# Optimization experiments

Measured on AMD Instinct MI355X. Metric: run time of the kernel, lower is better.

The kernel has to match this reference:

```python
import jax, jax.numpy as jnp
import numpy as np

DIM = 768
H = 12
D = DIM // H  # head_dim = 64
SCALE = D ** -0.5


def _split_heads(x):
    # [b, n, h*d] -> [b, h, n, d]
    b, n, _ = x.shape
    return x.reshape(b, n, H, D).transpose(0, 2, 1, 3)


def setup_inputs() -> dict:
    key = jax.random.key(0)
    ks = jax.random.split(key, 16)
    B, NQ, NKV = 2, 2048, 2048
    w_init = lambda k: jax.random.normal(k, (DIM, DIM), dtype=jnp.float32) * 0.02
    return {
        "words": jax.random.normal(ks[0], (B, NQ, DIM), dtype=jnp.float32),
        "position_words": jax.random.normal(ks[1], (B, NQ, DIM), dtype=jnp.float32),
        "conscious_words": jax.random.normal(ks[2], (B, NQ, DIM), dtype=jnp.float32),
        "cross_kv": jax.random.normal(ks[3], (B, NKV, DIM), dtype=jnp.float32),
        "position_cross": jax.random.normal(ks[4], (B, NKV, DIM), dtype=jnp.float32),
        "Wq_w": w_init(ks[5]), "Wk_w": w_init(ks[6]), "Wv_w": w_init(ks[7]),
        "Wq_p": w_init(ks[8]), "Wk_p": w_init(ks[9]),
        "Wq_c": w_init(ks[10]), "Wk_c": w_init(ks[11]),
        "latent_k": jax.random.normal(ks[12], (DIM,), dtype=jnp.float32),
        "Wo": w_init(ks[13]),
        "bo": jnp.zeros((DIM,), dtype=jnp.float32),
    }


def reference(words, position_words, conscious_words, cross_kv, position_cross,
              Wq_w, Wk_w, Wv_w, Wq_p, Wk_p, Wq_c, Wk_c, latent_k, Wo, bo):
    # Queries from three sources. Sum of the 9 pairwise QK^T scores equals
    # (sum of Qs) @ (sum of Ks)^T by bilinearity of matmul (same math as source).
    q = _split_heads(words @ Wq_w) + _split_heads(position_words @ Wq_p) \
        + _split_heads(conscious_words @ Wq_c)        # [b,h,nq,d]
    # latent conscious key: same vector for every kv position
    kc = (latent_k @ Wk_c).reshape(H, D)              # [h,d]
    k = _split_heads(cross_kv @ Wk_w) + _split_heads(position_cross @ Wk_p) \
        + kc[None, :, None, :]                        # [b,h,nkv,d]
    v = _split_heads(cross_kv @ Wv_w)                 # [b,h,nkv,d]

    score = jnp.einsum('bhid,bhjd->bhij', q, k) * SCALE  # [b,h,nq,nkv]
    attn = jax.nn.softmax(score, axis=-1)
    out = jnp.einsum('bhij,bhjd->bhid', attn, v)      # [b,h,nq,d]
    b, _, nq, _ = out.shape
    out = out.transpose(0, 2, 1, 3).reshape(b, nq, H * D)
    return out @ Wo + bo
```

## Files before the change

### kernel.cpp

```cpp
#include <hip/hip_runtime.h>
#include <math.h>

#define DIM  768
#define NH   12
#define HD   64
#define NQ   2048
#define NKV  2048
#define QSC_LOG2E 0.18033688011112042f

typedef short bf16x8  __attribute__((ext_vector_type(8)));
typedef float f32x4   __attribute__((ext_vector_type(4)));
typedef float f32x16  __attribute__((ext_vector_type(16)));

__device__ __forceinline__ unsigned short f2bf(float f) {
    unsigned u = __float_as_uint(f);
    unsigned r = (u + 0x7FFFu + ((u >> 16) & 1u)) >> 16;
    return (unsigned short)r;
}
__device__ __forceinline__ float bf2f(unsigned short u) {
    return __uint_as_float(((unsigned)u) << 16);
}

__device__ __forceinline__ unsigned cvtpk_bf16(float a, float b) {
    unsigned r;
    asm("v_cvt_pk_bf16_f32 %0, %1, %2" : "=v"(r) : "v"(a), "v"(b));
    return r;
}

__device__ __forceinline__ void plswap(unsigned& a, unsigned& b) {
    asm("v_permlane32_swap_b32 %0, %1" : "+v"(a), "+v"(b));
}

__device__ __forceinline__ float vexp2f(float x) {
#if __has_builtin(__builtin_amdgcn_exp2f)
    return __builtin_amdgcn_exp2f(x);
#else
    float r;
    asm("v_exp_f32 %0, %1\ns_nop 0" : "=v"(r) : "v"(x));
    return r;
#endif
}

__device__ __forceinline__ void ld_lds16(void* lds, const void* g) {
    __builtin_amdgcn_global_load_lds(
        (const __attribute__((address_space(1))) unsigned int*)g,
        (__attribute__((address_space(3))) unsigned int*)lds, 16, 0, 0);
}

__device__ __forceinline__ f32x16 z16() {
    f32x16 r;
    #pragma unroll
    for (int e = 0; e < 16; ++e) r[e] = 0.f;
    return r;
}

union PB16 { unsigned u[4]; bf16x8 v; };

__global__ __launch_bounds__(256)
void prep_kernel(const float* __restrict__ w0, const float* __restrict__ w1,
                 const float* __restrict__ w2, const float* __restrict__ w3,
                 const float* __restrict__ w4, const float* __restrict__ w5,
                 const float* __restrict__ w6, unsigned short* __restrict__ wt,
                 const float* __restrict__ latent, const float* __restrict__ Wkc,
                 float* __restrict__ kc) {
    __shared__ float t[32][33];
    int bid = blockIdx.x;
    if (bid < 4032) {
        int iz = bid / 576, rem = bid - iz * 576;
        int iy = rem / 24, ix = rem - iy * 24;
        const float* Ws[7] = {w0, w1, w2, w3, w4, w5, w6};
        const float* W = Ws[iz];
        unsigned short* D = wt + (size_t)iz * (768 * 768);
        int r0 = iy * 32, c0 = ix * 32;
        int tx = threadIdx.x & 31, ty = threadIdx.x >> 5;
        #pragma unroll
        for (int yy = 0; yy < 4; ++yy)
            t[ty * 4 + yy][tx] = W[(size_t)(r0 + ty * 4 + yy) * 768 + c0 + tx];
        __syncthreads();
        #pragma unroll
        for (int yy = 0; yy < 4; ++yy)
            D[(size_t)(c0 + ty * 4 + yy) * 768 + r0 + tx] = f2bf(t[tx][ty * 4 + yy]);
    } else {
        int jb = bid - 4032;
        float (&red)[16][17] = *reinterpret_cast<float(*)[16][17]>(&t[0][0]);
        int tx = threadIdx.x & 15, ty = threadIdx.x >> 4;
        int j = jb * 16 + tx;
        float acc = 0.f;
        for (int i = ty * 48; i < ty * 48 + 48; ++i)
            acc += latent[i] * Wkc[i * DIM + j];
        red[ty][tx] = acc;
        __syncthreads();
        if (ty == 0) {
            float s = 0.f;
            #pragma unroll
            for (int k = 0; k < 16; ++k) s += red[k][tx];
            kc[j] = s;
        }
    }
}

struct QCfg {
    const float* A0; const float* A1; const float* A2;
    const unsigned short* B0; const unsigned short* B1; const unsigned short* B2;
    const float* bias; float scale; void* out; int npair; int mode;
};

__global__ __launch_bounds__(256)
void gemm_qvk(QCfg c0, QCfg c1, QCfg c2) {
    __shared__ unsigned short As[2][64 * 64];
    __shared__ unsigned short Bs[2][128 * 64];
    const int tid = threadIdx.x;
    const int w = tid >> 6, l = tid & 63, g = l >> 4, r16 = l & 15;

    int p = blockIdx.x;
    int xcd = p & 7, s = p >> 3;
    int bx = s % 6, gg = s / 6;
    int gidx = gg * 8 + xcd;
    int by = gidx & 63, z = gidx >> 6;
    const int n0 = bx * 128, m0 = by * 64;

    QCfg c = (z == 0) ? c0 : (z == 1) ? c1 : c2;
    const float* Alist[3] = {c.A0, c.A1, c.A2};
    const unsigned short* Blist[3] = {c.B0, c.B1, c.B2};

    const int ar = tid >> 2, ac = (tid & 3) * 16;
    const int aswz = (ar & 7) << 4;
    float4 av0, av1, av2, av3;

    f32x4 acc[4][2];
    #pragma unroll
    for (int i = 0; i < 4; ++i)
        #pragma unroll
        for (int j = 0; j < 2; ++j) acc[i][j] = (f32x4){0.f, 0.f, 0.f, 0.f};

#define ALOAD(AP, K0) { \
    const float* _ap = (AP) + (size_t)(m0 + ar) * 768 + (K0) + ac; \
    av0 = *(const float4*)_ap;       av1 = *(const float4*)(_ap + 4); \
    av2 = *(const float4*)(_ap + 8); av3 = *(const float4*)(_ap + 12); }

#define AWRITE(BUFI) { \
    uint4 u0_, u1_; \
    u0_.x = cvtpk_bf16(av0.x, av0.y); u0_.y = cvtpk_bf16(av0.z, av0.w); \
    u0_.z = cvtpk_bf16(av1.x, av1.y); u0_.w = cvtpk_bf16(av1.z, av1.w); \
    u1_.x = cvtpk_bf16(av2.x, av2.y); u1_.y = cvtpk_bf16(av2.z, av2.w); \
    u1_.z = cvtpk_bf16(av3.x, av3.y); u1_.w = cvtpk_bf16(av3.z, av3.w); \
    *(uint4*)((char*)As[BUFI] + ar * 128 + ((2 * ac) ^ aswz)) = u0_; \
    *(uint4*)((char*)As[BUFI] + ar * 128 + ((2 * ac + 16) ^ aswz)) = u1_; }

#define BSTAGE(BUFI, BP, K0) { _Pragma("unroll") \
    for (int is = 0; is < 4; ++is) { \
        int u = is * 256 + tid, r = u >> 3, cc = u & 7; \
        int col = ((cc ^ (r & 7)) << 3); \
        ld_lds16((char*)Bs[BUFI] + is * 4096 + w * 1024, \
                 (BP) + (size_t)(n0 + r) * 768 + (K0) + col); } }

    const int NSTEPS = c.npair * 12;
    int pn = 0, kn = 0;
    ALOAD(Alist[0], 0);
    BSTAGE(0, Blist[0], 0);
    AWRITE(0);
    kn = 64;
    __syncthreads();

    #pragma unroll 1
    for (int st = 0; st < NSTEPS; ++st) {
        int cur = st & 1;
        bool pre = (st + 1 < NSTEPS);
        if (pre) {
            ALOAD(Alist[pn], kn);
            BSTAGE(cur ^ 1, Blist[pn], kn);
        }
        const char* Ab = (const char*)As[cur];
        const char* Bb = (const char*)Bs[cur];
        #pragma unroll
        for (int kk = 0; kk < 2; ++kk) {
            bf16x8 af[4], bf[2];
            #pragma unroll
            for (int i = 0; i < 4; ++i) {
                int row = i * 16 + r16;
                af[i] = *(const bf16x8*)(Ab + row * 128 +
                          ((kk * 64 + g * 16) ^ ((row & 7) << 4)));
            }
            #pragma unroll
            for (int j = 0; j < 2; ++j) {
                int row = w * 32 + j * 16 + r16;
                bf[j] = *(const bf16x8*)(Bb + row * 128 +
                          ((kk * 64 + g * 16) ^ ((row & 7) << 4)));
            }
            #pragma unroll
            for (int i = 0; i < 4; ++i)
                #pragma unroll
                for (int j = 0; j < 2; ++j)
                    acc[i][j] = __builtin_amdgcn_mfma_f32_16x16x32_bf16(
                        af[i], bf[j], acc[i][j], 0, 0, 0);
        }
        if (pre) {
            AWRITE(cur ^ 1);
            kn += 64; if (kn == 768) { kn = 0; ++pn; }
        }
        __syncthreads();
    }
#undef ALOAD
#undef AWRITE
#undef BSTAGE

    const int mode = c.mode;
    #pragma unroll
    for (int i = 0; i < 4; ++i) {
        #pragma unroll
        for (int j = 0; j < 2; ++j) {
            int col = n0 + w * 32 + j * 16 + r16;
            float bv = (mode == 0 && c.bias) ? c.bias[col] : 0.f;
            #pragma unroll
            for (int rr = 0; rr < 4; ++rr) {
                int row = m0 + i * 16 + g * 4 + rr;
                float v = acc[i][j][rr];
                if (mode == 2) v *= c.scale;
                v += bv;
                if (mode == 3) {
                    int bb = row >> 11, q = row & 2047;
                    ((unsigned short*)c.out)[(size_t)(bb * 768 + col) * 2048 + q] = f2bf(v);
                } else {
                    ((unsigned short*)c.out)[(size_t)row * 768 + col] = f2bf(v);
                }
            }
        }
    }
}

__global__ __launch_bounds__(256)
void gemm_out(const unsigned short* __restrict__ A,
              const unsigned short* __restrict__ B,
              const float* __restrict__ bias, float* __restrict__ Cout) {
    __shared__ unsigned short As[2][64 * 64];
    __shared__ unsigned short Bs[2][128 * 64];
    const int tid = threadIdx.x;
    const int w = tid >> 6, l = tid & 63, g = l >> 4, r16 = l & 15;

    int o_lin = blockIdx.x;
    int wl = (o_lin & 7) * 48 + (o_lin >> 3);
    int bx = wl % 6, by = wl / 6;
    const int n0 = bx * 128, m0 = by * 64;

    f32x4 acc[4][2];
    #pragma unroll
    for (int i = 0; i < 4; ++i)
        #pragma unroll
        for (int j = 0; j < 2; ++j) acc[i][j] = (f32x4){0.f, 0.f, 0.f, 0.f};

#define GSTAGE(BUFI, K0) { \
    _Pragma("unroll") \
    for (int is = 0; is < 2; ++is) { \
        int u = is * 256 + tid, r = u >> 3, cc = u & 7; \
        int col = ((cc ^ (r & 7)) << 3); \
        ld_lds16((char*)As[BUFI] + is * 4096 + w * 1024, \
                 A + (size_t)(m0 + r) * 768 + (K0) + col); } \
    _Pragma("unroll") \
    for (int is = 0; is < 4; ++is) { \
        int u = is * 256 + tid, r = u >> 3, cc = u & 7; \
        int col = ((cc ^ (r & 7)) << 3); \
        ld_lds16((char*)Bs[BUFI] + is * 4096 + w * 1024, \
                 B + (size_t)(n0 + r) * 768 + (K0) + col); } }

    GSTAGE(0, 0);
    __syncthreads();

    #pragma unroll 1
    for (int st = 0; st < 12; ++st) {
        int cur = st & 1;
        if (st + 1 < 12) GSTAGE(cur ^ 1, (st + 1) * 64);
        const char* Ab = (const char*)As[cur];
        const char* Bb = (const char*)Bs[cur];
        #pragma unroll
        for (int kk = 0; kk < 2; ++kk) {
            bf16x8 af[4], bf[2];
            #pragma unroll
            for (int i = 0; i < 4; ++i) {
                int row = i * 16 + r16;
                af[i] = *(const bf16x8*)(Ab + row * 128 +
                          ((kk * 64 + g * 16) ^ ((row & 7) << 4)));
            }
            #pragma unroll
            for (int j = 0; j < 2; ++j) {
                int row = w * 32 + j * 16 + r16;
                bf[j] = *(const bf16x8*)(Bb + row * 128 +
                          ((kk * 64 + g * 16) ^ ((row & 7) << 4)));
            }
            #pragma unroll
            for (int i = 0; i < 4; ++i)
                #pragma unroll
                for (int j = 0; j < 2; ++j)
                    acc[i][j] = __builtin_amdgcn_mfma_f32_16x16x32_bf16(
                        af[i], bf[j], acc[i][j], 0, 0, 0);
        }
        __syncthreads();
    }
#undef GSTAGE

    #pragma unroll
    for (int i = 0; i < 4; ++i) {
        #pragma unroll
        for (int j = 0; j < 2; ++j) {
            int col = n0 + w * 32 + j * 16 + r16;
            float bv = bias[col];
            #pragma unroll
            for (int rr = 0; rr < 4; ++rr) {
                int row = m0 + i * 16 + g * 4 + rr;
                Cout[(size_t)row * 768 + col] = acc[i][j][rr] + bv;
            }
        }
    }
}

__global__ __launch_bounds__(256)
void flash2(const unsigned short* __restrict__ Qb,
            const unsigned short* __restrict__ Kb,
            const unsigned short* __restrict__ Vt,
            unsigned short* __restrict__ P0, unsigned short* __restrict__ P1,
            unsigned short* __restrict__ P2, unsigned short* __restrict__ P3,
            float2* __restrict__ ML) {
    __shared__ unsigned short KV[2][2][4096];
    const int tid = threadIdx.x;
    const int w = tid >> 6, l = tid & 63, lo = l & 31, hi = l >> 5;

    int p = blockIdx.x + 64 * blockIdx.y;
    int xcd = p & 7, s = p >> 3;
    int gg = s >> 6, inner = s & 63;
    int bh = gg * 8 + xcd;
    int qi = inner >> 2, part = inner & 3;
    int b = bh / NH, h = bh % NH;
    int q0 = qi * 128;
    int kvbase = part * 512;

    bf16x8 qf[4];
    {
        const unsigned short* Qrow =
            Qb + (size_t)(b * NQ + q0 + w * 32 + lo) * DIM + h * HD + hi * 8;
        #pragma unroll
        for (int kc = 0; kc < 4; ++kc) qf[kc] = *(const bf16x8*)(Qrow + kc * 16);
    }

    f32x16 o0 = z16(), o1 = z16();
    float m = -3.0e38f, lsum = 0.f;

    const unsigned short* Kbase = Kb + (size_t)(b * NKV) * DIM + h * HD;
    const unsigned short* Vbase = Vt + ((size_t)b * DIM + h * HD) * NKV;

#define FSTAGE(BUFI, T0) { \
    _Pragma("unroll") \
    for (int is = 0; is < 2; ++is) { \
        int u = is * 256 + tid, r = u >> 3, cc = u & 7; \
        int col = ((cc ^ (r & 7)) << 3); \
        ld_lds16((char*)KV[BUFI][0] + is * 4096 + w * 1024, \
                 Kbase + (size_t)((T0) + r) * 768 + col); \
        ld_lds16((char*)KV[BUFI][1] + is * 4096 + w * 1024, \
                 Vbase + (size_t)r * 2048 + (T0) + col); } }

    FSTAGE(0, kvbase);
    __syncthreads();

    #pragma unroll 1
    for (int t = 0; t < 8; ++t) {
        int cur = t & 1;
        if (t < 7) FSTAGE(cur ^ 1, kvbase + (t + 1) * 64);

        const char* Kp = (const char*)KV[cur][0];
        const char* Vp = (const char*)KV[cur][1];

        f32x16 s0 = z16(), s1 = z16();
        __builtin_amdgcn_s_setprio(1);
        #pragma unroll
        for (int kc = 0; kc < 4; ++kc) {
            int r0 = lo, r1 = 32 + lo;
            bf16x8 k0 = *(const bf16x8*)(Kp + r0 * 128 +
                          ((kc * 32 + hi * 16) ^ ((r0 & 7) << 4)));
            bf16x8 k1 = *(const bf16x8*)(Kp + r1 * 128 +
                          ((kc * 32 + hi * 16) ^ ((r1 & 7) << 4)));
            s0 = __builtin_amdgcn_mfma_f32_32x32x16_bf16(k0, qf[kc], s0, 0, 0, 0);
            s1 = __builtin_amdgcn_mfma_f32_32x32x16_bf16(k1, qf[kc], s1, 0, 0, 0);
        }
        __builtin_amdgcn_s_setprio(0);

        float a8[8];
        #pragma unroll
        for (int e = 0; e < 8; ++e)
            a8[e] = fmaxf(fmaxf(fmaxf(s0[e], s0[e + 8]), s1[e]), s1[e + 8]);
        float pm = fmaxf(fmaxf(fmaxf(fmaxf(a8[0], a8[1]), fmaxf(a8[2], a8[3])),
                               fmaxf(fmaxf(a8[4], a8[5]), fmaxf(a8[6], a8[7]))), -3.0e38f);
        pm = fmaxf(pm, __shfl_xor(pm, 32));

        if (__any(pm > m + 10.f)) {
            float mn = fmaxf(m, pm);
            float sc = vexp2f(m - mn);
            lsum *= sc;
            #pragma unroll
            for (int e = 0; e < 16; ++e) { o0[e] *= sc; o1[e] *= sc; }
            m = mn;
        }

        #pragma unroll
        for (int e = 0; e < 16; ++e) {
            s0[e] = vexp2f(s0[e] - m);
            s1[e] = vexp2f(s1[e] - m);
        }

        float b8[8];
        #pragma unroll
        for (int e = 0; e < 8; ++e)
            b8[e] = (s0[e] + s0[e + 8]) + (s1[e] + s1[e + 8]);
        float rs = ((b8[0] + b8[1]) + (b8[2] + b8[3])) +
                   ((b8[4] + b8[5]) + (b8[6] + b8[7]));
        rs += __shfl_xor(rs, 32);
        lsum += rs;

        PB16 pb[4];
        #pragma unroll
        for (int cc = 0; cc < 2; ++cc) {
            unsigned a0 = cvtpk_bf16(s0[cc * 8 + 0], s0[cc * 8 + 1]);
            unsigned a1 = cvtpk_bf16(s0[cc * 8 + 2], s0[cc * 8 + 3]);
            unsigned b0 = cvtpk_bf16(s0[cc * 8 + 4], s0[cc * 8 + 5]);
            unsigned b1 = cvtpk_bf16(s0[cc * 8 + 6], s0[cc * 8 + 7]);
            plswap(a0, b0);
            plswap(a1, b1);
            pb[cc].u[0] = a0; pb[cc].u[1] = a1; pb[cc].u[2] = b0; pb[cc].u[3] = b1;
            unsigned c0 = cvtpk_bf16(s1[cc * 8 + 0], s1[cc * 8 + 1]);
            unsigned c1 = cvtpk_bf16(s1[cc * 8 + 2], s1[cc * 8 + 3]);
            unsigned d0 = cvtpk_bf16(s1[cc * 8 + 4], s1[cc * 8 + 5]);
            unsigned d1 = cvtpk_bf16(s1[cc * 8 + 6], s1[cc * 8 + 7]);
            plswap(c0, d0);
            plswap(c1, d1);
            pb[2 + cc].u[0] = c0; pb[2 + cc].u[1] = c1;
            pb[2 + cc].u[2] = d0; pb[2 + cc].u[3] = d1;
        }

        __builtin_amdgcn_s_setprio(1);
        #pragma unroll
        for (int c = 0; c < 4; ++c) {
            int r0 = lo, r1 = 32 + lo;
            bf16x8 v0 = *(const bf16x8*)(Vp + r0 * 128 +
                          ((c * 32 + hi * 16) ^ ((r0 & 7) << 4)));
            bf16x8 v1 = *(const bf16x8*)(Vp + r1 * 128 +
                          ((c * 32 + hi * 16) ^ ((r1 & 7) << 4)));
            o0 = __builtin_amdgcn_mfma_f32_32x32x16_bf16(v0, pb[c].v, o0, 0, 0, 0);
            o1 = __builtin_amdgcn_mfma_f32_32x32x16_bf16(v1, pb[c].v, o1, 0, 0, 0);
        }
        __builtin_amdgcn_s_setprio(0);
        __syncthreads();
    }
#undef FSTAGE

    unsigned short* Pp = (part == 0) ? P0 : (part == 1) ? P1 : (part == 2) ? P2 : P3;
    const int q = q0 + w * 32 + lo;
    unsigned short* Op = Pp + ((size_t)bh * 2048 + q) * 64;
    #pragma unroll
    for (int grp = 0; grp < 4; ++grp) {
        int r0 = grp * 4;
        int d0 = grp * 8 + 4 * hi;
        uint2 v0, v1;
        v0.x = cvtpk_bf16(o0[r0 + 0], o0[r0 + 1]);
        v0.y = cvtpk_bf16(o0[r0 + 2], o0[r0 + 3]);
        *(uint2*)(Op + d0) = v0;
        v1.x = cvtpk_bf16(o1[r0 + 0], o1[r0 + 1]);
        v1.y = cvtpk_bf16(o1[r0 + 2], o1[r0 + 3]);
        *(uint2*)(Op + 32 + d0) = v1;
    }
    if (hi == 0)
        ML[(size_t)(part * 24 + bh) * 2048 + q] = make_float2(m, lsum);
}

__global__ __launch_bounds__(256)
void combine4(const unsigned short* __restrict__ P0, const unsigned short* __restrict__ P1,
              const unsigned short* __restrict__ P2, const unsigned short* __restrict__ P3,
              const float2* __restrict__ ML, unsigned short* __restrict__ AO) {
    int bh = blockIdx.y;
    int idx = blockIdx.x * 256 + threadIdx.x;
    int q = idx >> 1, dh = (idx & 1) * 32;

    float2 u0 = ML[(size_t)(0 * 24 + bh) * 2048 + q];
    float2 u1 = ML[(size_t)(1 * 24 + bh) * 2048 + q];
    float2 u2 = ML[(size_t)(2 * 24 + bh) * 2048 + q];
    float2 u3 = ML[(size_t)(3 * 24 + bh) * 2048 + q];
    float M = fmaxf(fmaxf(u0.x, u1.x), fmaxf(u2.x, u3.x));
    float w0 = vexp2f(u0.x - M), w1 = vexp2f(u1.x - M);
    float w2 = vexp2f(u2.x - M), w3 = vexp2f(u3.x - M);
    float inv = 1.f / (w0 * u0.y + w1 * u1.y + w2 * u2.y + w3 * u3.y);
    w0 *= inv; w1 *= inv; w2 *= inv; w3 *= inv;

    size_t off = ((size_t)bh * 2048 + q) * 64 + dh;
    float acc[32];
    #pragma unroll
    for (int e = 0; e < 32; ++e) acc[e] = 0.f;
    const unsigned short* Ps[4] = {P0, P1, P2, P3};
    float ws[4] = {w0, w1, w2, w3};
    #pragma unroll
    for (int pp = 0; pp < 4; ++pp) {
        const unsigned short* src = Ps[pp] + off;
        float wv = ws[pp];
        #pragma unroll
        for (int c = 0; c < 4; ++c) {
            ushort4 hh2;
            uint4 vv = *(const uint4*)(src + c * 8);
            unsigned uu[4] = {vv.x, vv.y, vv.z, vv.w};
            #pragma unroll
            for (int e = 0; e < 4; ++e) {
                acc[c * 8 + e * 2 + 0] += wv * bf2f((unsigned short)(uu[e] & 0xFFFF));
                acc[c * 8 + e * 2 + 1] += wv * bf2f((unsigned short)(uu[e] >> 16));
            }
            (void)hh2;
        }
    }
    int b = bh / NH, h = bh % NH;
    unsigned short* dst = AO + ((size_t)(b * 2048 + q)) * DIM + h * HD + dh;
    #pragma unroll
    for (int c = 0; c < 4; ++c) {
        uint4 ov;
        ov.x = cvtpk_bf16(acc[c * 8 + 0], acc[c * 8 + 1]);
        ov.y = cvtpk_bf16(acc[c * 8 + 2], acc[c * 8 + 3]);
        ov.z = cvtpk_bf16(acc[c * 8 + 4], acc[c * 8 + 5]);
        ov.w = cvtpk_bf16(acc[c * 8 + 6], acc[c * 8 + 7]);
        *(uint4*)(dst + c * 8) = ov;
    }
}

extern "C" void kernel_launch(void* const* d_in, const int* in_sizes, int n_in,
                              void* d_out, int out_size, void* d_ws, size_t ws_size,
                              hipStream_t stream) {
    const float* words   = (const float*)d_in[0];
    const float* posw    = (const float*)d_in[1];
    const float* consc   = (const float*)d_in[2];
    const float* cross   = (const float*)d_in[3];
    const float* pcross  = (const float*)d_in[4];
    const float* Wq_w    = (const float*)d_in[5];
    const float* Wk_w    = (const float*)d_in[6];
    const float* Wv_w    = (const float*)d_in[7];
    const float* Wq_p    = (const float*)d_in[8];
    const float* Wk_p    = (const float*)d_in[9];
    const float* Wq_c    = (const float*)d_in[10];
    const float* Wk_c    = (const float*)d_in[11];
    const float* latentk = (const float*)d_in[12];
    const float* Wo      = (const float*)d_in[13];
    const float* bo      = (const float*)d_in[14];

    char* arena = (char*)d_ws;
    const size_t WTE = 768 * 768;
    unsigned short* WT = (unsigned short*)(arena);
    unsigned short* QB = (unsigned short*)(arena + 8257536);
    unsigned short* VT = (unsigned short*)(arena + 14548992);
    unsigned short* KB = (unsigned short*)(arena + 20840448);
    unsigned short* P0 = (unsigned short*)(arena + 27131904);
    unsigned short* P1 = (unsigned short*)(arena + 33423360);
    unsigned short* P2 = (unsigned short*)(arena + 39714816);
    unsigned short* P3 = (unsigned short*)(arena);
    float2* ML         = (float2*)(arena + 46006272);
    float* KCV         = (float*)(arena + 47579136);

    prep_kernel<<<dim3(4080), dim3(256), 0, stream>>>(
        Wq_w, Wq_p, Wq_c, Wk_w, Wk_p, Wv_w, Wo, WT, latentk, Wk_c, KCV);

    QCfg cq = { words, posw, consc,
                WT + 0 * WTE, WT + 1 * WTE, WT + 2 * WTE,
                nullptr, QSC_LOG2E, QB, 3, 2 };
    QCfg cv = { cross, nullptr, nullptr,
                WT + 5 * WTE, nullptr, nullptr,
                nullptr, 1.f, VT, 1, 3 };
    QCfg ck = { cross, pcross, nullptr,
                WT + 3 * WTE, WT + 4 * WTE, nullptr,
                KCV, 1.f, KB, 2, 0 };
    gemm_qvk<<<dim3(1152), dim3(256), 0, stream>>>(cq, cv, ck);

    flash2<<<dim3(64, 24), dim3(256), 0, stream>>>(QB, KB, VT, P0, P1, P2, P3, ML);

    combine4<<<dim3(16, 24), dim3(256), 0, stream>>>(P0, P1, P2, P3, ML, QB);

    gemm_out<<<dim3(384), dim3(256), 0, stream>>>(QB, WT + 6 * WTE, bo, (float*)d_out);
}
```

Baseline: 140.0 us.

## Enlarge projection GEMM tiles to 128x128 and drop LDS double buffering

Both the QKV projection and output projection GEMMs now use 128x128 block tiles, with a 2x2 wave arrangement where each wave computes a 64x64 sub-tile. This halves the block count and raises MFMA work per LDS load. Double buffering is replaced by single-buffered load/sync/compute steps with launch bounds set for occupancy 3. The mode-3 transposed V store is vectorised into uint2 writes. The trade-off is less load/compute overlap inside a block and fewer blocks per GPU (576 and 192), which risks underfilling the CUs.

After: 186.0 us. 32.8% more time.

```diff
diff --git a/kernel.cpp b/kernel.cpp
--- a/kernel.cpp
+++ b/kernel.cpp
@@ -105,209 +105,201 @@
     const float* bias; float scale; void* out; int npair; int mode;
 };
 
-__global__ __launch_bounds__(256)
+__global__ __launch_bounds__(256, 3)
 void gemm_qvk(QCfg c0, QCfg c1, QCfg c2) {
-    __shared__ unsigned short As[2][64 * 64];
-    __shared__ unsigned short Bs[2][128 * 64];
+    __shared__ unsigned short As[128 * 64];
+    __shared__ unsigned short Bs[128 * 64];
     const int tid = threadIdx.x;
     const int w = tid >> 6, l = tid & 63, g = l >> 4, r16 = l & 15;
+    const int wr = w >> 1, wc = w & 1;
 
     int p = blockIdx.x;
     int xcd = p & 7, s = p >> 3;
     int bx = s % 6, gg = s / 6;
     int gidx = gg * 8 + xcd;
-    int by = gidx & 63, z = gidx >> 6;
-    const int n0 = bx * 128, m0 = by * 64;
+    int by = gidx & 31, z = gidx >> 5;
+    const int n0 = bx * 128, m0 = by * 128;
 
     QCfg c = (z == 0) ? c0 : (z == 1) ? c1 : c2;
     const float* Alist[3] = {c.A0, c.A1, c.A2};
     const unsigned short* Blist[3] = {c.B0, c.B1, c.B2};
 
-    const int ar = tid >> 2, ac = (tid & 3) * 16;
+    const int ar = tid >> 1, ac = (tid & 1) * 32;
     const int aswz = (ar & 7) << 4;
-    float4 av0, av1, av2, av3;
-
-    f32x4 acc[4][2];
+
+    f32x4 acc[4][4];
     #pragma unroll
     for (int i = 0; i < 4; ++i)
         #pragma unroll
-        for (int j = 0; j < 2; ++j) acc[i][j] = (f32x4){0.f, 0.f, 0.f, 0.f};
-
-#define ALOAD(AP, K0) { \
-    const float* _ap = (AP) + (size_t)(m0 + ar) * 768 + (K0) + ac; \
-    av0 = *(const float4*)_ap;       av1 = *(const float4*)(_ap + 4); \
-    av2 = *(const float4*)(_ap + 8); av3 = *(const float4*)(_ap + 12); }
-
-#define AWRITE(BUFI) { \
-    uint4 u0_, u1_; \
-    u0_.x = cvtpk_bf16(av0.x, av0.y); u0_.y = cvtpk_bf16(av0.z, av0.w); \
-    u0_.z = cvtpk_bf16(av1.x, av1.y); u0_.w = cvtpk_bf16(av1.z, av1.w); \
-    u1_.x = cvtpk_bf16(av2.x, av2.y); u1_.y = cvtpk_bf16(av2.z, av2.w); \
-    u1_.z = cvtpk_bf16(av3.x, av3.y); u1_.w = cvtpk_bf16(av3.z, av3.w); \
-    *(uint4*)((char*)As[BUFI] + ar * 128 + ((2 * ac) ^ aswz)) = u0_; \
-    *(uint4*)((char*)As[BUFI] + ar * 128 + ((2 * ac + 16) ^ aswz)) = u1_; }
-
-#define BSTAGE(BUFI, BP, K0) { _Pragma("unroll") \
-    for (int is = 0; is < 4; ++is) { \
-        int u = is * 256 + tid, r = u >> 3, cc = u & 7; \
-        int col = ((cc ^ (r & 7)) << 3); \
-        ld_lds16((char*)Bs[BUFI] + is * 4096 + w * 1024, \
-                 (BP) + (size_t)(n0 + r) * 768 + (K0) + col); } }
+        for (int j = 0; j < 4; ++j) acc[i][j] = (f32x4){0.f, 0.f, 0.f, 0.f};
 
     const int NSTEPS = c.npair * 12;
     int pn = 0, kn = 0;
-    ALOAD(Alist[0], 0);
-    BSTAGE(0, Blist[0], 0);
-    AWRITE(0);
-    kn = 64;
-    __syncthreads();
 
     #pragma unroll 1
     for (int st = 0; st < NSTEPS; ++st) {
-        int cur = st & 1;
-        bool pre = (st + 1 < NSTEPS);
-        if (pre) {
-            ALOAD(Alist[pn], kn);
-            BSTAGE(cur ^ 1, Blist[pn], kn);
-        }
-        const char* Ab = (const char*)As[cur];
-        const char* Bb = (const char*)Bs[cur];
+        const float* Ap = Alist[pn] + (size_t)(m0 + ar) * 768 + kn + ac;
+        float4 av0 = *(const float4*)(Ap + 0);
+        float4 av1 = *(const float4*)(Ap + 4);
+        float4 av2 = *(const float4*)(Ap + 8);
+        float4 av3 = *(const float4*)(Ap + 12);
+        float4 av4 = *(const float4*)(Ap + 16);
+        float4 av5 = *(const float4*)(Ap + 20);
+        float4 av6 = *(const float4*)(Ap + 24);
+        float4 av7 = *(const float4*)(Ap + 28);
+        __syncthreads();
+        {
+            uint4 u0, u1, u2, u3;
+            u0.x = cvtpk_bf16(av0.x, av0.y); u0.y = cvtpk_bf16(av0.z, av0.w);
+            u0.z = cvtpk_bf16(av1.x, av1.y); u0.w = cvtpk_bf16(av1.z, av1.w);
+            u1.x = cvtpk_bf16(av2.x, av2.y); u1.y = cvtpk_bf16(av2.z, av2.w);
+            u1.z = cvtpk_bf16(av3.x, av3.y); u1.w = cvtpk_bf16(av3.z, av3.w);
+            u2.x = cvtpk_bf16(av4.x, av4.y); u2.y = cvtpk_bf16(av4.z, av4.w);
+            u2.z = cvtpk_bf16(av5.x, av5.y); u2.w = cvtpk_bf16(av5.z, av5.w);
+            u3.x = cvtpk_bf16(av6.x, av6.y); u3.y = cvtpk_bf16(av6.z, av6.w);
+            u3.z = cvtpk_bf16(av7.x, av7.y); u3.w = cvtpk_bf16(av7.z, av7.w);
+            char* dst = (char*)As + ar * 128;
+            *(uint4*)(dst + ((2 * ac + 0)  ^ aswz)) = u0;
+            *(uint4*)(dst + ((2 * ac + 16) ^ aswz)) = u1;
+            *(uint4*)(dst + ((2 * ac + 32) ^ aswz)) = u2;
+            *(uint4*)(dst + ((2 * ac + 48) ^ aswz)) = u3;
+        }
+        {
+            const unsigned short* Bp = Blist[pn];
+            #pragma unroll
+            for (int is = 0; is < 4; ++is) {
+                int u = is * 256 + tid, r = u >> 3, cc = u & 7;
+                int col = ((cc ^ (r & 7)) << 3);
+                ld_lds16((char*)Bs + is * 4096 + w * 1024,
+                         Bp + (size_t)(n0 + r) * 768 + kn + col);
+            }
+        }
+        __syncthreads();
+
         #pragma unroll
         for (int kk = 0; kk < 2; ++kk) {
-            bf16x8 af[4], bf[2];
+            bf16x8 af[4], bf[4];
             #pragma unroll
             for (int i = 0; i < 4; ++i) {
-                int row = i * 16 + r16;
-                af[i] = *(const bf16x8*)(Ab + row * 128 +
+                int row = wr * 64 + i * 16 + r16;
+                af[i] = *(const bf16x8*)((const char*)As + row * 128 +
                           ((kk * 64 + g * 16) ^ ((row & 7) << 4)));
             }
             #pragma unroll
-            for (int j = 0; j < 2; ++j) {
-                int row = w * 32 + j * 16 + r16;
-                bf[j] = *(const bf16x8*)(Bb + row * 128 +
+            for (int j = 0; j < 4; ++j) {
+                int row = wc * 64 + j * 16 + r16;
+                bf[j] = *(const bf16x8*)((const char*)Bs + row * 128 +
                           ((kk * 64 + g * 16) ^ ((row & 7) << 4)));
             }
             #pragma unroll
             for (int i = 0; i < 4; ++i)
                 #pragma unroll
-                for (int j = 0; j < 2; ++j)
+                for (int j = 0; j < 4; ++j)
                     acc[i][j] = __builtin_amdgcn_mfma_f32_16x16x32_bf16(
                         af[i], bf[j], acc[i][j], 0, 0, 0);
         }
-        if (pre) {
-            AWRITE(cur ^ 1);
-            kn += 64; if (kn == 768) { kn = 0; ++pn; }
-        }
-        __syncthreads();
-    }
-#undef ALOAD
-#undef AWRITE
-#undef BSTAGE
+        kn += 64; if (kn == 768) { kn = 0; ++pn; }
+    }
 
     const int mode = c.mode;
     #pragma unroll
     for (int i = 0; i < 4; ++i) {
         #pragma unroll
-        for (int j = 0; j < 2; ++j) {
-            int col = n0 + w * 32 + j * 16 + r16;
-            float bv = (mode == 0 && c.bias) ? c.bias[col] : 0.f;
-            #pragma unroll
-            for (int rr = 0; rr < 4; ++rr) {
-                int row = m0 + i * 16 + g * 4 + rr;
-                float v = acc[i][j][rr];
-                if (mode == 2) v *= c.scale;
-                v += bv;
-                if (mode == 3) {
-                    int bb = row >> 11, q = row & 2047;
-                    ((unsigned short*)c.out)[(size_t)(bb * 768 + col) * 2048 + q] = f2bf(v);
-                } else {
-                    ((unsigned short*)c.out)[(size_t)row * 768 + col] = f2bf(v);
+        for (int j = 0; j < 4; ++j) {
+            int col = n0 + wc * 64 + j * 16 + r16;
+            int row0 = m0 + wr * 64 + i * 16 + g * 4;
+            if (mode == 3) {
+                int bb = row0 >> 11, q = row0 & 2047;
+                uint2 v;
+                v.x = cvtpk_bf16(acc[i][j][0], acc[i][j][1]);
+                v.y = cvtpk_bf16(acc[i][j][2], acc[i][j][3]);
+                *(uint2*)((unsigned short*)c.out +
+                          (size_t)(bb * 768 + col) * 2048 + q) = v;
+            } else {
+                float bv = (mode == 0 && c.bias) ? c.bias[col] : 0.f;
+                #pragma unroll
+                for (int rr = 0; rr < 4; ++rr) {
+                    float v = acc[i][j][rr];
+                    if (mode == 2) v *= c.scale;
+                    v += bv;
+                    ((unsigned short*)c.out)[(size_t)(row0 + rr) * 768 + col] = f2bf(v);
                 }
             }
         }
     }
 }
 
-__global__ __launch_bounds__(256)
+__global__ __launch_bounds__(256, 3)
 void gemm_out(const unsigned short* __restrict__ A,
               const unsigned short* __restrict__ B,
               const float* __restrict__ bias, float* __restrict__ Cout) {
-    __shared__ unsigned short As[2][64 * 64];
-    __shared__ unsigned short Bs[2][128 * 64];
+    __shared__ unsigned short As[128 * 64];
+    __shared__ unsigned short Bs[128 * 64];
     const int tid = threadIdx.x;
     const int w = tid >> 6, l = tid & 63, g = l >> 4, r16 = l & 15;
-
-    int o_lin = blockIdx.x;
-    int wl = (o_lin & 7) * 48 + (o_lin >> 3);
-    int bx = wl % 6, by = wl / 6;
-    const int n0 = bx * 128, m0 = by * 64;
-
-    f32x4 acc[4][2];
+    const int wr = w >> 1, wc = w & 1;
+
+    int p = blockIdx.x;
+    int xcd = p & 7, s = p >> 3;
+    int bx = s % 6;
+    int by = (s / 6) * 8 + xcd;
+    const int n0 = bx * 128, m0 = by * 128;
+
+    f32x4 acc[4][4];
     #pragma unroll
     for (int i = 0; i < 4; ++i)
         #pragma unroll
-        for (int j = 0; j < 2; ++j) acc[i][j] = (f32x4){0.f, 0.f, 0.f, 0.f};
-
-#define GSTAGE(BUFI, K0) { \
-    _Pragma("unroll") \
-    for (int is = 0; is < 2; ++is) { \
-        int u = is * 256 + tid, r = u >> 3, cc = u & 7; \
-        int col = ((cc ^ (r & 7)) << 3); \
-        ld_lds16((char*)As[BUFI] + is * 4096 + w * 1024, \
-                 A + (size_t)(m0 + r) * 768 + (K0) + col); } \
-    _Pragma("unroll") \
-    for (int is = 0; is < 4; ++is) { \
-        int u = is * 256 + tid, r = u >> 3, cc = u & 7; \
-        int col = ((cc ^ (r & 7)) << 3); \
-        ld_lds16((char*)Bs[BUFI] + is * 4096 + w * 1024, \
-                 B + (size_t)(n0 + r) * 768 + (K0) + col); } }
-
-    GSTAGE(0, 0);
-    __syncthreads();
+        for (int j = 0; j < 4; ++j) acc[i][j] = (f32x4){0.f, 0.f, 0.f, 0.f};
 
     #pragma unroll 1
     for (int st = 0; st < 12; ++st) {
-        int cur = st & 1;
-        if (st + 1 < 12) GSTAGE(cur ^ 1, (st + 1) * 64);
-        const char* Ab = (const char*)As[cur];
-        const char* Bb = (const char*)Bs[cur];
+        int k0 = st * 64;
+        __syncthreads();
+        #pragma unroll
+        for (int is = 0; is < 4; ++is) {
+            int u = is * 256 + tid, r = u >> 3, cc = u & 7;
+            int col = ((cc ^ (r & 7)) << 3);
+            ld_lds16((char*)As + is * 4096 + w * 1024,
+                     A + (size_t)(m0 + r) * 768 + k0 + col);
+            ld_lds16((char*)Bs + is * 4096 + w * 1024,
+                     B + (size_t)(n0 + r) * 768 + k0 + col);
+        }
+        __syncthreads();
+
         #pragma unroll
         for (int kk = 0; kk < 2; ++kk) {
-            bf16x8 af[4], bf[2];
+            bf16x8 af[4], bf[4];
             #pragma unroll
             for (int i = 0; i < 4; ++i) {
-                int row = i * 16 + r16;
-                af[i] = *(const bf16x8*)(Ab + row * 128 +
+                int row = wr * 64 + i * 16 + r16;
+                af[i] = *(const bf16x8*)((const char*)As + row * 128 +
                           ((kk * 64 + g * 16) ^ ((row & 7) << 4)));
             }
             #pragma unroll
-            for (int j = 0; j < 2; ++j) {
-                int row = w * 32 + j * 16 + r16;
-                bf[j] = *(const bf16x8*)(Bb + row * 128 +
+            for (int j = 0; j < 4; ++j) {
+                int row = wc * 64 + j * 16 + r16;
+                bf[j] = *(const bf16x8*)((const char*)Bs + row * 128 +
                           ((kk * 64 + g * 16) ^ ((row & 7) << 4)));
             }
             #pragma unroll
             for (int i = 0; i < 4; ++i)
                 #pragma unroll
-                for (int j = 0; j < 2; ++j)
+                for (int j = 0; j < 4; ++j)
                     acc[i][j] = __builtin_amdgcn_mfma_f32_16x16x32_bf16(
                         af[i], bf[j], acc[i][j], 0, 0, 0);
         }
-        __syncthreads();
-    }
-#undef GSTAGE
+    }
 
     #pragma unroll
     for (int i = 0; i < 4; ++i) {
         #pragma unroll
-        for (int j = 0; j < 2; ++j) {
-            int col = n0 + w * 32 + j * 16 + r16;
+        for (int j = 0; j < 4; ++j) {
+            int col = n0 + wc * 64 + j * 16 + r16;
             float bv = bias[col];
-            #pragma unroll
-            for (int rr = 0; rr < 4; ++rr) {
-                int row = m0 + i * 16 + g * 4 + rr;
-                Cout[(size_t)row * 768 + col] = acc[i][j][rr] + bv;
-            }
+            int row0 = m0 + wr * 64 + i * 16 + g * 4;
+            #pragma unroll
+            for (int rr = 0; rr < 4; ++rr)
+                Cout[(size_t)(row0 + rr) * 768 + col] = acc[i][j][rr] + bv;
         }
     }
 }
@@ -385,8 +377,8 @@
         #pragma unroll
         for (int e = 0; e < 8; ++e)
             a8[e] = fmaxf(fmaxf(fmaxf(s0[e], s0[e + 8]), s1[e]), s1[e + 8]);
-        float pm = fmaxf(fmaxf(fmaxf(fmaxf(a8[0], a8[1]), fmaxf(a8[2], a8[3])),
-                               fmaxf(fmaxf(a8[4], a8[5]), fmaxf(a8[6], a8[7]))), -3.0e38f);
+        float pm = fmaxf(fmaxf(fmaxf(a8[0], a8[1]), fmaxf(a8[2], a8[3])),
+                         fmaxf(fmaxf(a8[4], a8[5]), fmaxf(a8[6], a8[7])));
         pm = fmaxf(pm, __shfl_xor(pm, 32));
 
         if (__any(pm > m + 10.f)) {
@@ -498,7 +490,6 @@
         float wv = ws[pp];
         #pragma unroll
         for (int c = 0; c < 4; ++c) {
-            ushort4 hh2;
             uint4 vv = *(const uint4*)(src + c * 8);
             unsigned uu[4] = {vv.x, vv.y, vv.z, vv.w};
             #pragma unroll
@@ -506,7 +497,6 @@
                 acc[c * 8 + e * 2 + 0] += wv * bf2f((unsigned short)(uu[e] & 0xFFFF));
                 acc[c * 8 + e * 2 + 1] += wv * bf2f((unsigned short)(uu[e] >> 16));
             }
-            (void)hh2;
         }
     }
     int b = bh / NH, h = bh % NH;
@@ -566,11 +556,11 @@
     QCfg ck = { cross, pcross, nullptr,
                 WT + 3 * WTE, WT + 4 * WTE, nullptr,
                 KCV, 1.f, KB, 2, 0 };
-    gemm_qvk<<<dim3(1152), dim3(256), 0, stream>>>(cq, cv, ck);
+    gemm_qvk<<<dim3(576), dim3(256), 0, stream>>>(cq, cv, ck);
 
     flash2<<<dim3(64, 24), dim3(256), 0, stream>>>(QB, KB, VT, P0, P1, P2, P3, ML);
 
     combine4<<<dim3(16, 24), dim3(256), 0, stream>>>(P0, P1, P2, P3, ML, QB);
 
-    gemm_out<<<dim3(384), dim3(256), 0, stream>>>(QB, WT + 6 * WTE, bo, (float*)d_out);
-}
+    gemm_out<<<dim3(192), dim3(256), 0, stream>>>(QB, WT + 6 * WTE, bo, (float*)d_out);
+}
```

## Restructure QKV projection GEMM main loop into unrolled two-stage pipeline with explicit waits

Applied to the files above, without the earlier changes.

The QKV projection GEMM loop is rewritten as a manually unrolled pair of steps. The fp32 A tiles now load into two alternating register sets, so A can be fetched one extra step ahead. The single __syncthreads is replaced with fine-grained s_waitcnt vmcnt/lgkmcnt plus s_barrier, so some outstanding global loads can stay in flight across the barrier. A launch-bounds occupancy hint of 3 is added, and a redundant clamp in the attention max reduction is dropped. The trade-offs are more registers for the duplicate A buffers and reliance on hand-counted vmcnt values being correct.

After: 142.1 us, median of 3. About the same (+1.5%).

```diff
diff --git a/kernel.cpp b/kernel.cpp
--- a/kernel.cpp
+++ b/kernel.cpp
@@ -105,7 +105,7 @@
     const float* bias; float scale; void* out; int npair; int mode;
 };
 
-__global__ __launch_bounds__(256)
+__global__ __launch_bounds__(256, 3)
 void gemm_qvk(QCfg c0, QCfg c1, QCfg c2) {
     __shared__ unsigned short As[2][64 * 64];
     __shared__ unsigned short Bs[2][128 * 64];
@@ -125,7 +125,6 @@
 
     const int ar = tid >> 2, ac = (tid & 3) * 16;
     const int aswz = (ar & 7) << 4;
-    float4 av0, av1, av2, av3;
 
     f32x4 acc[4][2];
     #pragma unroll
@@ -133,76 +132,96 @@
         #pragma unroll
         for (int j = 0; j < 2; ++j) acc[i][j] = (f32x4){0.f, 0.f, 0.f, 0.f};
 
-#define ALOAD(AP, K0) { \
-    const float* _ap = (AP) + (size_t)(m0 + ar) * 768 + (K0) + ac; \
-    av0 = *(const float4*)_ap;       av1 = *(const float4*)(_ap + 4); \
-    av2 = *(const float4*)(_ap + 8); av3 = *(const float4*)(_ap + 12); }
-
-#define AWRITE(BUFI) { \
-    uint4 u0_, u1_; \
-    u0_.x = cvtpk_bf16(av0.x, av0.y); u0_.y = cvtpk_bf16(av0.z, av0.w); \
-    u0_.z = cvtpk_bf16(av1.x, av1.y); u0_.w = cvtpk_bf16(av1.z, av1.w); \
-    u1_.x = cvtpk_bf16(av2.x, av2.y); u1_.y = cvtpk_bf16(av2.z, av2.w); \
-    u1_.z = cvtpk_bf16(av3.x, av3.y); u1_.w = cvtpk_bf16(av3.z, av3.w); \
-    *(uint4*)((char*)As[BUFI] + ar * 128 + ((2 * ac) ^ aswz)) = u0_; \
-    *(uint4*)((char*)As[BUFI] + ar * 128 + ((2 * ac + 16) ^ aswz)) = u1_; }
-
-#define BSTAGE(BUFI, BP, K0) { _Pragma("unroll") \
+    const int NSTEPS = c.npair * 12;
+    int pnA = 0, knA = 0;
+    int pnB = 0, knB = 0;
+    float4 xa0, xa1, xa2, xa3;
+    float4 ya0, ya1, ya2, ya3;
+
+#define ALOADX { const float* _ap = Alist[pnA] + (size_t)(m0 + ar) * 768 + knA + ac; \
+    xa0 = *(const float4*)_ap;       xa1 = *(const float4*)(_ap + 4); \
+    xa2 = *(const float4*)(_ap + 8); xa3 = *(const float4*)(_ap + 12); \
+    knA += 64; if (knA == 768) { knA = 0; ++pnA; } }
+#define ALOADY { const float* _ap = Alist[pnA] + (size_t)(m0 + ar) * 768 + knA + ac; \
+    ya0 = *(const float4*)_ap;       ya1 = *(const float4*)(_ap + 4); \
+    ya2 = *(const float4*)(_ap + 8); ya3 = *(const float4*)(_ap + 12); \
+    knA += 64; if (knA == 768) { knA = 0; ++pnA; } }
+#define AWR(BUFI, v0, v1, v2, v3) { uint4 u0_, u1_; \
+    u0_.x = cvtpk_bf16(v0.x, v0.y); u0_.y = cvtpk_bf16(v0.z, v0.w); \
+    u0_.z = cvtpk_bf16(v1.x, v1.y); u0_.w = cvtpk_bf16(v1.z, v1.w); \
+    u1_.x = cvtpk_bf16(v2.x, v2.y); u1_.y = cvtpk_bf16(v2.z, v2.w); \
+    u1_.z = cvtpk_bf16(v3.x, v3.y); u1_.w = cvtpk_bf16(v3.z, v3.w); \
+    char* _dst = (char*)As[BUFI] + ar * 128; \
+    *(uint4*)(_dst + ((2 * ac) ^ aswz)) = u0_; \
+    *(uint4*)(_dst + ((2 * ac + 16) ^ aswz)) = u1_; }
+#define BSTG(BUFI) { const unsigned short* _bp = Blist[pnB]; \
+    _Pragma("unroll") \
     for (int is = 0; is < 4; ++is) { \
-        int u = is * 256 + tid, r = u >> 3, cc = u & 7; \
-        int col = ((cc ^ (r & 7)) << 3); \
+        int u = is * 256 + tid, r = u >> 3, cc2 = u & 7; \
+        int col = ((cc2 ^ (r & 7)) << 3); \
         ld_lds16((char*)Bs[BUFI] + is * 4096 + w * 1024, \
-                 (BP) + (size_t)(n0 + r) * 768 + (K0) + col); } }
-
-    const int NSTEPS = c.npair * 12;
-    int pn = 0, kn = 0;
-    ALOAD(Alist[0], 0);
-    BSTAGE(0, Blist[0], 0);
-    AWRITE(0);
-    kn = 64;
-    __syncthreads();
-
+                 _bp + (size_t)(n0 + r) * 768 + knB + col); } \
+    knB += 64; if (knB == 768) { knB = 0; ++pnB; } }
+#define COMPUTE(BUFI) { const char* Ab = (const char*)As[BUFI]; \
+    const char* Bb = (const char*)Bs[BUFI]; \
+    _Pragma("unroll") \
+    for (int kk = 0; kk < 2; ++kk) { \
+        bf16x8 af[4], bf[2]; \
+        _Pragma("unroll") \
+        for (int i = 0; i < 4; ++i) { int row = i * 16 + r16; \
+            af[i] = *(const bf16x8*)(Ab + row * 128 + ((kk * 64 + g * 16) ^ ((row & 7) << 4))); } \
+        _Pragma("unroll") \
+        for (int j = 0; j < 2; ++j) { int row = w * 32 + j * 16 + r16; \
+            bf[j] = *(const bf16x8*)(Bb + row * 128 + ((kk * 64 + g * 16) ^ ((row & 7) << 4))); } \
+        _Pragma("unroll") \
+        for (int i = 0; i < 4; ++i) \
+            _Pragma("unroll") \
+            for (int j = 0; j < 2; ++j) \
+                acc[i][j] = __builtin_amdgcn_mfma_f32_16x16x32_bf16( \
+                    af[i], bf[j], acc[i][j], 0, 0, 0); } }
+#define WAITV4 asm volatile("s_waitcnt vmcnt(4)" ::: "memory")
+#define WAITV0 asm volatile("s_waitcnt vmcnt(0)" ::: "memory")
+#define WAITL0 asm volatile("s_waitcnt lgkmcnt(0)" ::: "memory")
+
+    ALOADX;
+    BSTG(0);
+    ALOADY;
+    AWR(0, xa0, xa1, xa2, xa3);
+    WAITV4; WAITL0;
+    __builtin_amdgcn_s_barrier();
+
+    const int P = NSTEPS >> 1;
     #pragma unroll 1
-    for (int st = 0; st < NSTEPS; ++st) {
-        int cur = st & 1;
-        bool pre = (st + 1 < NSTEPS);
-        if (pre) {
-            ALOAD(Alist[pn], kn);
-            BSTAGE(cur ^ 1, Blist[pn], kn);
-        }
-        const char* Ab = (const char*)As[cur];
-        const char* Bb = (const char*)Bs[cur];
-        #pragma unroll
-        for (int kk = 0; kk < 2; ++kk) {
-            bf16x8 af[4], bf[2];
-            #pragma unroll
-            for (int i = 0; i < 4; ++i) {
-                int row = i * 16 + r16;
-                af[i] = *(const bf16x8*)(Ab + row * 128 +
-                          ((kk * 64 + g * 16) ^ ((row & 7) << 4)));
-            }
-            #pragma unroll
-            for (int j = 0; j < 2; ++j) {
-                int row = w * 32 + j * 16 + r16;
-                bf[j] = *(const bf16x8*)(Bb + row * 128 +
-                          ((kk * 64 + g * 16) ^ ((row & 7) << 4)));
-            }
-            #pragma unroll
-            for (int i = 0; i < 4; ++i)
-                #pragma unroll
-                for (int j = 0; j < 2; ++j)
-                    acc[i][j] = __builtin_amdgcn_mfma_f32_16x16x32_bf16(
-                        af[i], bf[j], acc[i][j], 0, 0, 0);
-        }
-        if (pre) {
-            AWRITE(cur ^ 1);
-            kn += 64; if (kn == 768) { kn = 0; ++pn; }
-        }
-        __syncthreads();
-    }
-#undef ALOAD
-#undef AWRITE
-#undef BSTAGE
+    for (int it = 0; it < P; ++it) {
+        const int st = it * 2;
+        BSTG(1);
+        const bool a2 = (st + 2 < NSTEPS);
+        if (a2) ALOADX;
+        COMPUTE(0);
+        AWR(1, ya0, ya1, ya2, ya3);
+        if (a2) { WAITV4; } else { WAITV0; }
+        WAITL0;
+        __builtin_amdgcn_s_barrier();
+        const bool b2 = (st + 2 < NSTEPS);
+        const bool a3 = (st + 3 < NSTEPS);
+        if (b2) BSTG(0);
+        if (a3) ALOADY;
+        COMPUTE(1);
+        if (b2) {
+            AWR(0, xa0, xa1, xa2, xa3);
+            if (a3) { WAITV4; } else { WAITV0; }
+            WAITL0;
+            __builtin_amdgcn_s_barrier();
+        }
+    }
+#undef ALOADX
+#undef ALOADY
+#undef AWR
+#undef BSTG
+#undef COMPUTE
+#undef WAITV4
+#undef WAITV0
+#undef WAITL0
 
     const int mode = c.mode;
     #pragma unroll
@@ -385,8 +404,8 @@
         #pragma unroll
         for (int e = 0; e < 8; ++e)
             a8[e] = fmaxf(fmaxf(fmaxf(s0[e], s0[e + 8]), s1[e]), s1[e + 8]);
-        float pm = fmaxf(fmaxf(fmaxf(fmaxf(a8[0], a8[1]), fmaxf(a8[2], a8[3])),
-                               fmaxf(fmaxf(a8[4], a8[5]), fmaxf(a8[6], a8[7]))), -3.0e38f);
+        float pm = fmaxf(fmaxf(fmaxf(a8[0], a8[1]), fmaxf(a8[2], a8[3])),
+                         fmaxf(fmaxf(a8[4], a8[5]), fmaxf(a8[6], a8[7])));
         pm = fmaxf(pm, __shfl_xor(pm, 32));
 
         if (__any(pm > m + 10.f)) {
@@ -498,7 +517,6 @@
         float wv = ws[pp];
         #pragma unroll
         for (int c = 0; c < 4; ++c) {
-            ushort4 hh2;
             uint4 vv = *(const uint4*)(src + c * 8);
             unsigned uu[4] = {vv.x, vv.y, vv.z, vv.w};
             #pragma unroll
@@ -506,7 +524,6 @@
                 acc[c * 8 + e * 2 + 0] += wv * bf2f((unsigned short)(uu[e] & 0xFFFF));
                 acc[c * 8 + e * 2 + 1] += wv * bf2f((unsigned short)(uu[e] >> 16));
             }
-            (void)hh2;
         }
     }
     int b = bh / NH, h = bh % NH;
```
